# Kernel tuning notes

Measured on AMD Instinct MI355X. Metric: run time of the kernel, lower is better.

Reference implementation:

```python
import jax, jax.numpy as jnp
import numpy as np

N_NODES = 50000
N_EDGES = 1600000
IN_DIM = 128
HID = 128
N_GRAPHS = 64
N_CLASSES = 1


def _seg_sum(x, ids, n):
    return jax.ops.segment_sum(x, ids, num_segments=n)


def _gcn_layer(h, W, b, src, dst, src_isqrt, dst_isqrt):
    # DGL GraphConv, norm='both': D_dst^{-1/2} A D_src^{-1/2} (h W) + b
    hw = h @ W                                  # [N, out]
    msg = (hw * src_isqrt[:, None])[src]        # gather -> [E, out]
    agg = _seg_sum(msg, dst, h.shape[0])        # scatter-add -> [N, out]
    return agg * dst_isqrt[:, None] + b


def setup_inputs() -> dict:
    key = jax.random.key(0)
    ks = jax.random.split(key, 16)
    x = jax.random.normal(ks[0], (N_NODES, IN_DIM), dtype=jnp.float32)
    src = jax.random.randint(ks[1], (N_EDGES,), 0, N_NODES)
    dst = jax.random.randint(ks[2], (N_EDGES,), 0, N_NODES)
    graph_id = jnp.sort(jax.random.randint(ks[3], (N_NODES,), 0, N_GRAPHS))
    s = 1.0 / np.sqrt(HID)
    params = {
        'W1': jax.random.uniform(ks[4], (IN_DIM, HID), jnp.float32, -s, s),
        'b1': jnp.zeros((HID,), jnp.float32),
        'W2': jax.random.uniform(ks[5], (HID, HID), jnp.float32, -s, s),
        'b2': jnp.zeros((HID,), jnp.float32),
        'Wc1': jax.random.uniform(ks[6], (HID, HID // 2), jnp.float32, -s, s),
        'bc1': jnp.zeros((HID // 2,), jnp.float32),
        'Wc2': jax.random.uniform(ks[7], (HID // 2, HID // 4), jnp.float32, -s, s),
        'bc2': jnp.zeros((HID // 4,), jnp.float32),
        'Wc3': jax.random.uniform(ks[8], (HID // 4, HID // 8), jnp.float32, -s, s),
        'bc3': jnp.zeros((HID // 8,), jnp.float32),
        'Wc4': jax.random.uniform(ks[9], (HID // 8, N_CLASSES), jnp.float32, -s, s),
        'bc4': jnp.zeros((N_CLASSES,), jnp.float32),
    }
    return dict(x=x, src=src, dst=dst, graph_id=graph_id, num_graphs=N_GRAPHS, **params)


def reference(x, src, dst, graph_id, num_graphs, W1, b1, W2, b2,
              Wc1, bc1, Wc2, bc2, Wc3, bc3, Wc4, bc4):
    n = x.shape[0]
    ones = jnp.ones((src.shape[0],), x.dtype)
    out_deg = jnp.clip(_seg_sum(ones, src, n), 1.0)
    in_deg = jnp.clip(_seg_sum(ones, dst, n), 1.0)
    src_isqrt = jax.lax.rsqrt(out_deg)
    dst_isqrt = jax.lax.rsqrt(in_deg)

    h = jax.nn.relu(_gcn_layer(x, W1, b1, src, dst, src_isqrt, dst_isqrt))
    h = jax.nn.relu(_gcn_layer(h, W2, b2, src, dst, src_isqrt, dst_isqrt))

    # dgl.mean_nodes: per-graph mean of node features
    sums = _seg_sum(h, graph_id, num_graphs)                       # [G, HID]
    cnts = jnp.clip(_seg_sum(jnp.ones((n,), h.dtype), graph_id, num_graphs), 1.0)
    hg = sums / cnts[:, None]

    o = jax.nn.relu(hg @ Wc1 + bc1)
    o = jax.nn.relu(o @ Wc2 + bc2)
    o = jax.nn.relu(o @ Wc3 + bc3)
    return o @ Wc4 + bc4
```

## Files before the change

### kernel.cpp

```cpp
#include <hip/hip_runtime.h>
#include <hip/hip_fp16.h>

#define FDIM 128
#define NGRAPH 64
#define POOL_CHUNK 64
#define CBLK 256
#define OCHUNK 6400
#define OBLK 64

typedef _Float16 f16;
typedef f16 f16x8 __attribute__((ext_vector_type(8)));
typedef float f32x4 __attribute__((ext_vector_type(4)));
typedef float f32x2 __attribute__((ext_vector_type(2)));

__device__ __forceinline__ int lower_bound_i(const int* a, int n, int v) {
    int lo = 0, hi = n;
    while (lo < hi) { int m = (lo + hi) >> 1; if (a[m] < v) lo = m + 1; else hi = m; }
    return lo;
}

__global__ __launch_bounds__(256) void k_pre(
        const float* __restrict__ W1, f16* __restrict__ W1h, f16* __restrict__ W1l,
        const float* __restrict__ W2, f16* __restrict__ W2h, f16* __restrict__ W2l,
        float* __restrict__ hg, const int* __restrict__ dst, int* __restrict__ partial,
        const int* __restrict__ src, int* __restrict__ out_part,
        int E, int N, int NBIN, int CE) {
    __shared__ int lds[OCHUNK];
    const int t = threadIdx.x;
    int b = blockIdx.x;
    if (b < 128) {
        int i = b * 256 + t;
        if (i < NGRAPH * FDIM) hg[i] = 0.f;
        int j = i & 16383;
        int k = j >> 7, n = j & 127;
        const float* W = (i < 16384) ? W1 : W2;
        f16* Wh = (i < 16384) ? W1h : W2h;
        f16* Wl = (i < 16384) ? W1l : W2l;
        float v = W[j];
        f16 hi = (f16)v;
        Wh[n * FDIM + k] = hi;
        Wl[n * FDIM + k] = (f16)(v - (float)hi);
    } else if (b < 128 + CBLK) {
        b -= 128;
        for (int i = t; i < 4 * 257; i += 256) lds[i] = 0;
        __syncthreads();
        const int wv = t >> 6;
        const int s = b * CE, e = min(E, s + CE);
        for (int i = s + t; i < e; i += 256)
            atomicAdd(&lds[wv * 257 + (dst[i] >> 8)], 1);
        __syncthreads();
        for (int i = t; i < NBIN; i += 256)
            partial[i * CBLK + b] = lds[i] + lds[257 + i] + lds[514 + i] + lds[771 + i];
    } else {
        b -= (128 + CBLK);
        const int c = b / OBLK, sl = b % OBLK;
        for (int i = t; i < OCHUNK; i += 256) lds[i] = 0;
        __syncthreads();
        const int lo = c * OCHUNK;
        const int SE = (E + OBLK - 1) / OBLK;
        const int s = sl * SE, e = min(E, s + SE);
        for (int i = s + t; i < e; i += 256) {
            int v = src[i] - lo;
            if ((unsigned)v < (unsigned)OCHUNK) atomicAdd(&lds[v], 1);
        }
        __syncthreads();
        const int hi = min(N - lo, OCHUNK);
        for (int i = t; i < hi; i += 256)
            out_part[(size_t)sl * N + lo + i] = lds[i];
    }
}

__global__ void k_scan1(const int* __restrict__ in, int* __restrict__ out,
                        int* __restrict__ bsum, int M) {
    __shared__ int s[256];
    int t = threadIdx.x;
    int i = blockIdx.x * 256 + t;
    int v = (i < M) ? in[i] : 0;
    s[t] = v;
    __syncthreads();
    for (int off = 1; off < 256; off <<= 1) {
        int x = (t >= off) ? s[t - off] : 0;
        __syncthreads();
        s[t] += x;
        __syncthreads();
    }
    if (i < M) out[i] = s[t] - v;
    if (t == 255) bsum[blockIdx.x] = s[t];
}

__global__ __launch_bounds__(256) void k_coarse_scatter(
        const int* __restrict__ src, const int* __restrict__ dst,
        const int* __restrict__ offs, const int* __restrict__ bsum,
        unsigned* __restrict__ coarse_buf, int E, int CE, int NBIN) {
    __shared__ int cur[256], sb[256];
    const int t = threadIdx.x, b = blockIdx.x;
    int v = (t < NBIN) ? bsum[t] : 0;
    sb[t] = v;
    __syncthreads();
    for (int off = 1; off < 256; off <<= 1) {
        int x = (t >= off) ? sb[t - off] : 0;
        __syncthreads();
        sb[t] += x;
        __syncthreads();
    }
    if (t < NBIN) cur[t] = offs[t * CBLK + b] + (sb[t] - v);
    __syncthreads();
    const int s = b * CE, e = min(E, s + CE);
    for (int i = s + t; i < e; i += 256) {
        int d = dst[i];
        int p = atomicAdd(&cur[d >> 8], 1);
        coarse_buf[p] = ((unsigned)d << 16) | (unsigned)src[i];
    }
}

__global__ __launch_bounds__(256) void k_fine(
        const unsigned* __restrict__ coarse_buf, const int* __restrict__ bsum,
        int* __restrict__ csr_src, int* __restrict__ row_ptr, int N, int E, int NBIN) {
    __shared__ int h[256], sc[256], cur[256];
    const int t = threadIdx.x, g = blockIdx.x;
    int bv = (t < NBIN) ? bsum[t] : 0;
    sc[t] = bv;
    __syncthreads();
    for (int off = 1; off < 256; off <<= 1) {
        int x = (t >= off) ? sc[t - off] : 0;
        __syncthreads();
        sc[t] += x;
        __syncthreads();
    }
    __syncthreads();
    if (t == 0) { h[0] = sc[g] - bsum[g]; h[1] = sc[g]; }
    __syncthreads();
    const int s = h[0], e = h[1];
    __syncthreads();
    h[t] = 0;
    __syncthreads();
    for (int i = s + t; i < e; i += 256)
        atomicAdd(&h[(coarse_buf[i] >> 16) & 255], 1);
    __syncthreads();
    int v = h[t];
    sc[t] = v;
    __syncthreads();
    for (int off = 1; off < 256; off <<= 1) {
        int x = (t >= off) ? sc[t - off] : 0;
        __syncthreads();
        sc[t] += x;
        __syncthreads();
    }
    const int excl = sc[t] - v;
    const int node = g * 256 + t;
    if (node < N) row_ptr[node] = s + excl;
    if (node == N) row_ptr[N] = s + excl;
    cur[t] = s + excl;
    __syncthreads();
    for (int i = s + t; i < e; i += 256) {
        unsigned p = coarse_buf[i];
        int f = (p >> 16) & 255;
        int pos = atomicAdd(&cur[f], 1);
        csr_src[pos] = (int)(p & 0xFFFFu);
    }
    if (g == NBIN - 1 && t == 0 && (N & 255) == 0) row_ptr[N] = E;
}

template<bool IN_F16>
__global__ __launch_bounds__(256) void k_gemm_mfma(
        const void* __restrict__ Xv, const f16* __restrict__ Wh,
        const f16* __restrict__ Wl, const int* __restrict__ out_part,
        float* __restrict__ sisq, unsigned char* __restrict__ out, int N) {
    __shared__ __align__(16) f16 smem[128 * 136];
    __shared__ float sisql[128];
    const int t = threadIdx.x;
    const int w = t >> 6;
    const int lane = t & 63;
    const int base = blockIdx.x * 128;

    if (t < 128) {
        int row = base + t;
        float sv = 1.f;
        if (row < N) {
            if (IN_F16) {
                sv = sisq[row];
            } else {
                int a = 0;
#pragma unroll
                for (int bb = 0; bb < OBLK; bb++) a += out_part[(size_t)bb * N + row];
                sv = rsqrtf((float)max(a, 1));
                sisq[row] = sv;
            }
        }
        sisql[t] = sv;
    }
    for (int i = t; i < 2048; i += 256) {
        int n = i >> 4, kc = (i & 15) * 8;
        *(uint4*)&smem[n * 136 + kc] = *(const uint4*)&Wh[n * FDIM + kc];
    }
    __syncthreads();

    const int mrow = lane & 15;
    const int kq = (lane >> 4) * 8;
    const int arow0 = min(base + w * 32 + mrow, N - 1);
    const int arow1 = min(base + w * 32 + 16 + mrow, N - 1);

    f16x8 a0[4], a1[4];
    if (IN_F16) {
        const f16* X = (const f16*)Xv;
#pragma unroll
        for (int kk = 0; kk < 4; kk++) {
            a0[kk] = *(const f16x8*)&X[(size_t)arow0 * FDIM + kk * 32 + kq];
            a1[kk] = *(const f16x8*)&X[(size_t)arow1 * FDIM + kk * 32 + kq];
        }
    } else {
        const float* X = (const float*)Xv;
#pragma unroll
        for (int kk = 0; kk < 4; kk++) {
            float4 u0 = *(const float4*)&X[(size_t)arow0 * FDIM + kk * 32 + kq];
            float4 u1 = *(const float4*)&X[(size_t)arow0 * FDIM + kk * 32 + kq + 4];
            float4 v0 = *(const float4*)&X[(size_t)arow1 * FDIM + kk * 32 + kq];
            float4 v1 = *(const float4*)&X[(size_t)arow1 * FDIM + kk * 32 + kq + 4];
            f16x8 av;
            av[0] = (f16)u0.x; av[1] = (f16)u0.y; av[2] = (f16)u0.z; av[3] = (f16)u0.w;
            av[4] = (f16)u1.x; av[5] = (f16)u1.y; av[6] = (f16)u1.z; av[7] = (f16)u1.w;
            a0[kk] = av;
            av[0] = (f16)v0.x; av[1] = (f16)v0.y; av[2] = (f16)v0.z; av[3] = (f16)v0.w;
            av[4] = (f16)v1.x; av[5] = (f16)v1.y; av[6] = (f16)v1.z; av[7] = (f16)v1.w;
            a1[kk] = av;
        }
    }

    f32x4 acc0[8], acc1[8];
#pragma unroll
    for (int nt = 0; nt < 8; nt++) {
        acc0[nt] = (f32x4){0.f, 0.f, 0.f, 0.f};
        acc1[nt] = (f32x4){0.f, 0.f, 0.f, 0.f};
    }

#pragma unroll
    for (int kk = 0; kk < 4; kk++) {
#pragma unroll
        for (int nt = 0; nt < 8; nt++) {
            f16x8 bh = *(const f16x8*)&smem[(nt * 16 + mrow) * 136 + kk * 32 + kq];
            f16x8 bl = *(const f16x8*)&Wl[(nt * 16 + mrow) * FDIM + kk * 32 + kq];
            acc0[nt] = __builtin_amdgcn_mfma_f32_16x16x32_f16(a0[kk], bh, acc0[nt], 0, 0, 0);
            acc1[nt] = __builtin_amdgcn_mfma_f32_16x16x32_f16(a1[kk], bh, acc1[nt], 0, 0, 0);
            acc0[nt] = __builtin_amdgcn_mfma_f32_16x16x32_f16(a0[kk], bl, acc0[nt], 0, 0, 0);
            acc1[nt] = __builtin_amdgcn_mfma_f32_16x16x32_f16(a1[kk], bl, acc1[nt], 0, 0, 0);
        }
    }

    const int r0 = (lane >> 4) * 4;
    float sv0[4], sv1[4];
#pragma unroll
    for (int j = 0; j < 4; j++) {
        sv0[j] = sisql[w * 32 + r0 + j];
        sv1[j] = sisql[w * 32 + 16 + r0 + j];
    }
    __syncthreads();
#pragma unroll
    for (int nt = 0; nt < 8; nt++) {
        int c = nt * 16 + mrow;
#pragma unroll
        for (int j = 0; j < 4; j++) {
            smem[(w * 32 + r0 + j) * 136 + c]      = (f16)(acc0[nt][j] * sv0[j]);
            smem[(w * 32 + 16 + r0 + j) * 136 + c] = (f16)(acc1[nt][j] * sv1[j]);
        }
    }
    __syncthreads();
    {
        int r = t >> 1, cb = (t & 1) * 64;
        int row = base + r;
        if (row < N) {
            unsigned char* dstp = out + (size_t)row * FDIM + cb;
#pragma unroll
            for (int g2 = 0; g2 < 4; g2++) {
                unsigned wv[4];
#pragma unroll
                for (int k2 = 0; k2 < 4; k2++) {
                    const f16* p = &smem[r * 136 + cb + g2 * 16 + k2 * 4];
                    int w0 = __builtin_amdgcn_cvt_pk_fp8_f32((float)p[0], (float)p[1], 0, false);
                    w0 = __builtin_amdgcn_cvt_pk_fp8_f32((float)p[2], (float)p[3], w0, true);
                    wv[k2] = (unsigned)w0;
                }
                uint4 u;
                u.x = wv[0]; u.y = wv[1]; u.z = wv[2]; u.w = wv[3];
                *(uint4*)&dstp[g2 * 16] = u;
            }
        }
    }
}

__device__ __forceinline__ void accF8(float* acc, uint2 v) {
    f32x2 a0 = __builtin_amdgcn_cvt_pk_f32_fp8((int)v.x, false);
    f32x2 a1 = __builtin_amdgcn_cvt_pk_f32_fp8((int)v.x, true);
    f32x2 a2 = __builtin_amdgcn_cvt_pk_f32_fp8((int)v.y, false);
    f32x2 a3 = __builtin_amdgcn_cvt_pk_f32_fp8((int)v.y, true);
    acc[0] += a0.x; acc[1] += a0.y; acc[2] += a1.x; acc[3] += a1.y;
    acc[4] += a2.x; acc[5] += a2.y; acc[6] += a3.x; acc[7] += a3.y;
}

__global__ __launch_bounds__(256) void k_aggregate(
        const unsigned char* __restrict__ hws, const int* __restrict__ csr_src,
        const int* __restrict__ row_ptr,
        const float* __restrict__ bias, f16* __restrict__ out, int N) {
    const int t = threadIdx.x;
    const int node = blockIdx.x * 16 + (t >> 4);
    if (node >= N) return;
    const int fbase = (t & 15) * 8;

    const int s = row_ptr[node];
    const int e = row_ptr[node + 1];
    float acc[8];
#pragma unroll
    for (int j = 0; j < 8; j++) acc[j] = 0.f;

    int i = s;
    for (; i + 8 <= e; i += 8) {
        int u[8];
#pragma unroll
        for (int j = 0; j < 8; j++) u[j] = csr_src[i + j];
        uint2 v[8];
#pragma unroll
        for (int j = 0; j < 8; j++)
            v[j] = *(const uint2*)(hws + (size_t)u[j] * FDIM + fbase);
#pragma unroll
        for (int j = 0; j < 8; j++) accF8(acc, v[j]);
    }
    if (i + 4 <= e) {
        int u[4];
#pragma unroll
        for (int j = 0; j < 4; j++) u[j] = csr_src[i + j];
        uint2 v[4];
#pragma unroll
        for (int j = 0; j < 4; j++)
            v[j] = *(const uint2*)(hws + (size_t)u[j] * FDIM + fbase);
#pragma unroll
        for (int j = 0; j < 4; j++) accF8(acc, v[j]);
        i += 4;
    }
    for (; i < e; i++) {
        int u = csr_src[i];
        uint2 v = *(const uint2*)(hws + (size_t)u * FDIM + fbase);
        accF8(acc, v);
    }

    const float d = rsqrtf((float)max(e - s, 1));
    f16 res[8];
#pragma unroll
    for (int j = 0; j < 8; j++)
        res[j] = (f16)fmaxf(fmaf(acc[j], d, bias[fbase + j]), 0.f);
    *(uint4*)(out + (size_t)node * FDIM + fbase) = *(const uint4*)res;
}

__global__ void k_pool_sum(const f16* __restrict__ h, const int* __restrict__ gid,
                           float* __restrict__ hg, int N) {
    const int t = threadIdx.x;
    int s = blockIdx.x * POOL_CHUNK;
    int e = min(N, s + POOL_CHUNK);
    if (s >= e) return;
    int g = gid[s];
    float acc = 0.f;
    for (int n = s; n < e; n++) {
        int gn = gid[n];
        if (gn != g) {
            atomicAdd(&hg[g * FDIM + t], acc);
            acc = 0.f;
            g = gn;
        }
        acc += (float)h[(size_t)n * FDIM + t];
    }
    atomicAdd(&hg[g * FDIM + t], acc);
}

__global__ __launch_bounds__(256) void k_mlp(
        const float* __restrict__ hg, const int* __restrict__ gid, int N,
        const float* __restrict__ Wc1, const float* __restrict__ bc1,
        const float* __restrict__ Wc2, const float* __restrict__ bc2,
        const float* __restrict__ Wc3, const float* __restrict__ bc3,
        const float* __restrict__ Wc4, const float* __restrict__ bc4,
        float* __restrict__ out) {
    __shared__ float A[NGRAPH * 128];
    __shared__ float O1[NGRAPH * 64];
    __shared__ float O2[NGRAPH * 32];
    __shared__ float O3[NGRAPH * 16];
    __shared__ float inv_cnt[NGRAPH];
    const int t = threadIdx.x;

    if (t < NGRAPH) {
        int s = lower_bound_i(gid, N, t);
        int e = lower_bound_i(gid, N, t + 1);
        inv_cnt[t] = 1.f / fmaxf((float)(e - s), 1.f);
    }
    __syncthreads();

    for (int i = t; i < NGRAPH * 128; i += 256) A[i] = hg[i] * inv_cnt[i >> 7];
    __syncthreads();

    for (int i = t; i < NGRAPH * 64; i += 256) {
        int g = i >> 6, o = i & 63;
        float a = bc1[o];
        for (int k = 0; k < 128; k++) a = fmaf(A[g * 128 + k], Wc1[k * 64 + o], a);
        O1[i] = fmaxf(a, 0.f);
    }
    __syncthreads();

    for (int i = t; i < NGRAPH * 32; i += 256) {
        int g = i >> 5, o = i & 31;
        float a = bc2[o];
        for (int k = 0; k < 64; k++) a = fmaf(O1[g * 64 + k], Wc2[k * 32 + o], a);
        O2[i] = fmaxf(a, 0.f);
    }
    __syncthreads();

    for (int i = t; i < NGRAPH * 16; i += 256) {
        int g = i >> 4, o = i & 15;
        float a = bc3[o];
        for (int k = 0; k < 32; k++) a = fmaf(O2[g * 32 + k], Wc3[k * 16 + o], a);
        O3[i] = fmaxf(a, 0.f);
    }
    __syncthreads();

    if (t < NGRAPH) {
        float a = bc4[0];
        for (int k = 0; k < 16; k++) a = fmaf(O3[t * 16 + k], Wc4[k], a);
        out[t] = a;
    }
}

extern "C" void kernel_launch(void* const* d_in, const int* in_sizes, int n_in,
                              void* d_out, int out_size, void* d_ws, size_t ws_size,
                              hipStream_t stream) {
    const float* x   = (const float*)d_in[0];
    const int*   src = (const int*)d_in[1];
    const int*   dst = (const int*)d_in[2];
    const int*   gid = (const int*)d_in[3];
    const float* W1  = (const float*)d_in[5];
    const float* b1  = (const float*)d_in[6];
    const float* W2  = (const float*)d_in[7];
    const float* b2  = (const float*)d_in[8];
    const float* Wc1 = (const float*)d_in[9];
    const float* bc1 = (const float*)d_in[10];
    const float* Wc2 = (const float*)d_in[11];
    const float* bc2 = (const float*)d_in[12];
    const float* Wc3 = (const float*)d_in[13];
    const float* bc3 = (const float*)d_in[14];
    const float* Wc4 = (const float*)d_in[15];
    const float* bc4 = (const float*)d_in[16];
    float* out = (float*)d_out;

    const int N = in_sizes[0] / FDIM;
    const int E = in_sizes[1];

    const int NBIN = (N + 255) >> 8;
    const int M    = NBIN * CBLK;
    const int CE   = (E + CBLK - 1) / CBLK;
    const int OC   = (N + OCHUNK - 1) / OCHUNK;

    char* w = (char*)d_ws;
    size_t off = 0;
    auto alloc = [&](size_t bytes) -> void* {
        void* p = w + off;
        off = (off + bytes + 255) & ~(size_t)255;
        return p;
    };
    unsigned char* hws = (unsigned char*)alloc((size_t)N * FDIM);
    f16*   h       = (f16*)   alloc((size_t)N * FDIM * 2);
    int*   csr_src = (int*)   alloc((size_t)E * 4);
    int*   partial = (int*)   alloc((size_t)M * 4);
    int*   offs    = (int*)   alloc((size_t)M * 4);
    int*   row_ptr = (int*)   alloc((size_t)(N + 1) * 4);
    float* sisq    = (float*) alloc((size_t)N * 4);
    int*   bsum    = (int*)   alloc(256 * 4);
    float* hg      = (float*) alloc(NGRAPH * FDIM * 4);
    f16*   W1t     = (f16*)   alloc(FDIM * FDIM * 2);
    f16*   W1l     = (f16*)   alloc(FDIM * FDIM * 2);
    f16*   W2t     = (f16*)   alloc(FDIM * FDIM * 2);
    f16*   W2l     = (f16*)   alloc(FDIM * FDIM * 2);
    unsigned* coarse_buf = (unsigned*)hws;
    int*      out_part   = (int*)h;

    k_pre<<<128 + CBLK + OC * OBLK, 256, 0, stream>>>(
        W1, W1t, W1l, W2, W2t, W2l, hg, dst, partial, src, out_part, E, N, NBIN, CE);
    k_scan1<<<NBIN, 256, 0, stream>>>(partial, offs, bsum, M);
    k_coarse_scatter<<<CBLK, 256, 0, stream>>>(src, dst, offs, bsum, coarse_buf, E, CE, NBIN);
    k_fine<<<NBIN, 256, 0, stream>>>(coarse_buf, bsum, csr_src, row_ptr, N, E, NBIN);

    const int gT = (N + 127) / 128;
    const int gA = (N + 15) / 16;

    k_gemm_mfma<false><<<gT, 256, 0, stream>>>(x, W1t, W1l, out_part, sisq, hws, N);
    k_aggregate<<<gA, 256, 0, stream>>>(hws, csr_src, row_ptr, b1, h, N);
    k_gemm_mfma<true><<<gT, 256, 0, stream>>>(h, W2t, W2l, nullptr, sisq, hws, N);
    k_aggregate<<<gA, 256, 0, stream>>>(hws, csr_src, row_ptr, b2, h, N);
    const int gP = (N + POOL_CHUNK - 1) / POOL_CHUNK;
    k_pool_sum<<<gP, 128, 0, stream>>>(h, gid, hg, N);
    k_mlp<<<1, 256, 0, stream>>>(hg, gid, N, Wc1, bc1, Wc2, bc2, Wc3, bc3, Wc4, bc4, out);
}
```

Measured before the change: 323.1 us.

## Merge fine CSR pass with first GEMM and move out-degree count into scan launch

Reorganises the preprocessing launch schedule. The out-degree histogram moves from the first preprocessing kernel into the scan kernel's launch, and the fine CSR bucketing runs in the same launch as the first-layer GEMM. Independent work now shares launches, which cuts kernel boundaries and lets the light fine/scan blocks overlap with heavier work. The cost is separate workspace buffers for coarse_buf and out_part instead of aliasing hws and h, plus a larger LDS footprint for the merged kernels, which may reduce occupancy.

```diff
diff --git a/kernel.cpp b/kernel.cpp
--- a/kernel.cpp
+++ b/kernel.cpp
@@ -23,9 +23,8 @@
         const float* __restrict__ W1, f16* __restrict__ W1h, f16* __restrict__ W1l,
         const float* __restrict__ W2, f16* __restrict__ W2h, f16* __restrict__ W2l,
         float* __restrict__ hg, const int* __restrict__ dst, int* __restrict__ partial,
-        const int* __restrict__ src, int* __restrict__ out_part,
-        int E, int N, int NBIN, int CE) {
-    __shared__ int lds[OCHUNK];
+        int E, int NBIN, int CE) {
+    __shared__ int lds[4 * 257];
     const int t = threadIdx.x;
     int b = blockIdx.x;
     if (b < 128) {
@@ -40,7 +39,7 @@
         f16 hi = (f16)v;
         Wh[n * FDIM + k] = hi;
         Wl[n * FDIM + k] = (f16)(v - (float)hi);
-    } else if (b < 128 + CBLK) {
+    } else {
         b -= 128;
         for (int i = t; i < 4 * 257; i += 256) lds[i] = 0;
         __syncthreads();
@@ -51,8 +50,31 @@
         __syncthreads();
         for (int i = t; i < NBIN; i += 256)
             partial[i * CBLK + b] = lds[i] + lds[257 + i] + lds[514 + i] + lds[771 + i];
+    }
+}
+
+__global__ __launch_bounds__(256) void k_scan_oh(
+        const int* __restrict__ partial, int* __restrict__ offs, int* __restrict__ bsum,
+        int M, const int* __restrict__ src, int* __restrict__ out_part,
+        int E, int N, int NBIN) {
+    __shared__ int lds[OCHUNK];
+    const int t = threadIdx.x;
+    int b = blockIdx.x;
+    if (b < NBIN) {
+        int i = b * 256 + t;
+        int v = (i < M) ? partial[i] : 0;
+        lds[t] = v;
+        __syncthreads();
+        for (int off = 1; off < 256; off <<= 1) {
+            int x = (t >= off) ? lds[t - off] : 0;
+            __syncthreads();
+            lds[t] += x;
+            __syncthreads();
+        }
+        if (i < M) offs[i] = lds[t] - v;
+        if (t == 255) bsum[b] = lds[t];
     } else {
-        b -= (128 + CBLK);
+        b -= NBIN;
         const int c = b / OBLK, sl = b % OBLK;
         for (int i = t; i < OCHUNK; i += 256) lds[i] = 0;
         __syncthreads();
@@ -68,24 +90,6 @@
         for (int i = t; i < hi; i += 256)
             out_part[(size_t)sl * N + lo + i] = lds[i];
     }
-}
-
-__global__ void k_scan1(const int* __restrict__ in, int* __restrict__ out,
-                        int* __restrict__ bsum, int M) {
-    __shared__ int s[256];
-    int t = threadIdx.x;
-    int i = blockIdx.x * 256 + t;
-    int v = (i < M) ? in[i] : 0;
-    s[t] = v;
-    __syncthreads();
-    for (int off = 1; off < 256; off <<= 1) {
-        int x = (t >= off) ? s[t - off] : 0;
-        __syncthreads();
-        s[t] += x;
-        __syncthreads();
-    }
-    if (i < M) out[i] = s[t] - v;
-    if (t == 255) bsum[blockIdx.x] = s[t];
 }
 
 __global__ __launch_bounds__(256) void k_coarse_scatter(
@@ -113,65 +117,16 @@
     }
 }
 
-__global__ __launch_bounds__(256) void k_fine(
-        const unsigned* __restrict__ coarse_buf, const int* __restrict__ bsum,
-        int* __restrict__ csr_src, int* __restrict__ row_ptr, int N, int E, int NBIN) {
-    __shared__ int h[256], sc[256], cur[256];
-    const int t = threadIdx.x, g = blockIdx.x;
-    int bv = (t < NBIN) ? bsum[t] : 0;
-    sc[t] = bv;
-    __syncthreads();
-    for (int off = 1; off < 256; off <<= 1) {
-        int x = (t >= off) ? sc[t - off] : 0;
-        __syncthreads();
-        sc[t] += x;
-        __syncthreads();
-    }
-    __syncthreads();
-    if (t == 0) { h[0] = sc[g] - bsum[g]; h[1] = sc[g]; }
-    __syncthreads();
-    const int s = h[0], e = h[1];
-    __syncthreads();
-    h[t] = 0;
-    __syncthreads();
-    for (int i = s + t; i < e; i += 256)
-        atomicAdd(&h[(coarse_buf[i] >> 16) & 255], 1);
-    __syncthreads();
-    int v = h[t];
-    sc[t] = v;
-    __syncthreads();
-    for (int off = 1; off < 256; off <<= 1) {
-        int x = (t >= off) ? sc[t - off] : 0;
-        __syncthreads();
-        sc[t] += x;
-        __syncthreads();
-    }
-    const int excl = sc[t] - v;
-    const int node = g * 256 + t;
-    if (node < N) row_ptr[node] = s + excl;
-    if (node == N) row_ptr[N] = s + excl;
-    cur[t] = s + excl;
-    __syncthreads();
-    for (int i = s + t; i < e; i += 256) {
-        unsigned p = coarse_buf[i];
-        int f = (p >> 16) & 255;
-        int pos = atomicAdd(&cur[f], 1);
-        csr_src[pos] = (int)(p & 0xFFFFu);
-    }
-    if (g == NBIN - 1 && t == 0 && (N & 255) == 0) row_ptr[N] = E;
-}
-
 template<bool IN_F16>
-__global__ __launch_bounds__(256) void k_gemm_mfma(
+__device__ __forceinline__ void gemm_body(
+        f16* smem, float* sisql, int blk,
         const void* __restrict__ Xv, const f16* __restrict__ Wh,
         const f16* __restrict__ Wl, const int* __restrict__ out_part,
         float* __restrict__ sisq, unsigned char* __restrict__ out, int N) {
-    __shared__ __align__(16) f16 smem[128 * 136];
-    __shared__ float sisql[128];
     const int t = threadIdx.x;
     const int w = t >> 6;
     const int lane = t & 63;
-    const int base = blockIdx.x * 128;
+    const int base = blk * 128;
 
     if (t < 128) {
         int row = base + t;
@@ -285,6 +240,75 @@
             }
         }
     }
+}
+
+__global__ __launch_bounds__(256) void k_fine_gemm(
+        const unsigned* __restrict__ coarse_buf, const int* __restrict__ bsum,
+        int* __restrict__ csr_src, int* __restrict__ row_ptr, int N, int E, int NBIN,
+        const float* __restrict__ x, const f16* __restrict__ Wh,
+        const f16* __restrict__ Wl, const int* __restrict__ out_part,
+        float* __restrict__ sisq, unsigned char* __restrict__ hws) {
+    __shared__ __align__(16) f16 smem[128 * 136];
+    __shared__ float sisql[128];
+    const int t = threadIdx.x;
+    const int g = blockIdx.x;
+    if (g >= NBIN) {
+        gemm_body<false>(smem, sisql, g - NBIN, x, Wh, Wl, out_part, sisq, hws, N);
+        return;
+    }
+    int* h  = (int*)smem;
+    int* sc = h + 256;
+    int* cur = h + 512;
+    int bv = (t < NBIN) ? bsum[t] : 0;
+    sc[t] = bv;
+    __syncthreads();
+    for (int off = 1; off < 256; off <<= 1) {
+        int xx = (t >= off) ? sc[t - off] : 0;
+        __syncthreads();
+        sc[t] += xx;
+        __syncthreads();
+    }
+    __syncthreads();
+    if (t == 0) { h[0] = sc[g] - bsum[g]; h[1] = sc[g]; }
+    __syncthreads();
+    const int s = h[0], e = h[1];
+    __syncthreads();
+    h[t] = 0;
+    __syncthreads();
+    for (int i = s + t; i < e; i += 256)
+        atomicAdd(&h[(coarse_buf[i] >> 16) & 255], 1);
+    __syncthreads();
+    int v = h[t];
+    sc[t] = v;
+    __syncthreads();
+    for (int off = 1; off < 256; off <<= 1) {
+        int xx = (t >= off) ? sc[t - off] : 0;
+        __syncthreads();
+        sc[t] += xx;
+        __syncthreads();
+    }
+    const int excl = sc[t] - v;
+    const int node = g * 256 + t;
+    if (node < N) row_ptr[node] = s + excl;
+    if (node == N) row_ptr[N] = s + excl;
+    cur[t] = s + excl;
+    __syncthreads();
+    for (int i = s + t; i < e; i += 256) {
+        unsigned p = coarse_buf[i];
+        int f = (p >> 16) & 255;
+        int pos = atomicAdd(&cur[f], 1);
+        csr_src[pos] = (int)(p & 0xFFFFu);
+    }
+    if (g == NBIN - 1 && t == 0 && (N & 255) == 0) row_ptr[N] = E;
+}
+
+__global__ __launch_bounds__(256) void k_gemm2(
+        const f16* __restrict__ X, const f16* __restrict__ Wh,
+        const f16* __restrict__ Wl, float* __restrict__ sisq,
+        unsigned char* __restrict__ out, int N) {
+    __shared__ __align__(16) f16 smem[128 * 136];
+    __shared__ float sisql[128];
+    gemm_body<true>(smem, sisql, blockIdx.x, X, Wh, Wl, nullptr, sisq, out, N);
 }
 
 __device__ __forceinline__ void accF8(float* acc, uint2 v) {
@@ -463,6 +487,8 @@
     unsigned char* hws = (unsigned char*)alloc((size_t)N * FDIM);
     f16*   h       = (f16*)   alloc((size_t)N * FDIM * 2);
     int*   csr_src = (int*)   alloc((size_t)E * 4);
+    unsigned* coarse_buf = (unsigned*)alloc((size_t)E * 4);
+    int*   out_part = (int*) alloc((size_t)OBLK * N * 4);
     int*   partial = (int*)   alloc((size_t)M * 4);
     int*   offs    = (int*)   alloc((size_t)M * 4);
     int*   row_ptr = (int*)   alloc((size_t)(N + 1) * 4);
@@ -473,21 +499,20 @@
     f16*   W1l     = (f16*)   alloc(FDIM * FDIM * 2);
     f16*   W2t     = (f16*)   alloc(FDIM * FDIM * 2);
     f16*   W2l     = (f16*)   alloc(FDIM * FDIM * 2);
-    unsigned* coarse_buf = (unsigned*)hws;
-    int*      out_part   = (int*)h;
-
-    k_pre<<<128 + CBLK + OC * OBLK, 256, 0, stream>>>(
-        W1, W1t, W1l, W2, W2t, W2l, hg, dst, partial, src, out_part, E, N, NBIN, CE);
-    k_scan1<<<NBIN, 256, 0, stream>>>(partial, offs, bsum, M);
-    k_coarse_scatter<<<CBLK, 256, 0, stream>>>(src, dst, offs, bsum, coarse_buf, E, CE, NBIN);
-    k_fine<<<NBIN, 256, 0, stream>>>(coarse_buf, bsum, csr_src, row_ptr, N, E, NBIN);
 
     const int gT = (N + 127) / 128;
     const int gA = (N + 15) / 16;
 
-    k_gemm_mfma<false><<<gT, 256, 0, stream>>>(x, W1t, W1l, out_part, sisq, hws, N);
+    k_pre<<<128 + CBLK, 256, 0, stream>>>(
+        W1, W1t, W1l, W2, W2t, W2l, hg, dst, partial, E, NBIN, CE);
+    k_scan_oh<<<NBIN + OC * OBLK, 256, 0, stream>>>(
+        partial, offs, bsum, M, src, out_part, E, N, NBIN);
+    k_coarse_scatter<<<CBLK, 256, 0, stream>>>(src, dst, offs, bsum, coarse_buf, E, CE, NBIN);
+    k_fine_gemm<<<NBIN + gT, 256, 0, stream>>>(
+        coarse_buf, bsum, csr_src, row_ptr, N, E, NBIN,
+        x, W1t, W1l, out_part, sisq, hws);
     k_aggregate<<<gA, 256, 0, stream>>>(hws, csr_src, row_ptr, b1, h, N);
-    k_gemm_mfma<true><<<gT, 256, 0, stream>>>(h, W2t, W2l, nullptr, sisq, hws, N);
+    k_gemm2<<<gT, 256, 0, stream>>>(h, W2t, W2l, sisq, hws, N);
     k_aggregate<<<gA, 256, 0, stream>>>(hws, csr_src, row_ptr, b2, h, N);
     const int gP = (N + POOL_CHUNK - 1) / POOL_CHUNK;
     k_pool_sum<<<gP, 128, 0, stream>>>(h, gid, hg, N);
```

New measurement: 312.8 us. -3.2%, faster.
